# Kernel optimization log

Hardware: AMD Instinct MI355X
Metric: run time of the kernel (lower is better)

Reference implementation:

```python
import jax, jax.numpy as jnp
import numpy as np

V, C, T_MAX, H, L = 32000, 256, 2048, 8, 4
HS = C // H          # head_size = 32
FFN = 256            # hard-coded in Encoder
CLS_H, N_OUT = 512, 10
B, T = 4, 2048
EPS = 1e-5


def _ln(x, g, b):
    mu = jnp.mean(x, axis=-1, keepdims=True)
    var = jnp.mean(jnp.square(x - mu), axis=-1, keepdims=True)
    return (x - mu) * jax.lax.rsqrt(var + EPS) * g + b


def setup_inputs() -> dict:
    key = jax.random.key(0)
    ks = jax.random.split(key, 16)
    s = 0.02
    return {
        "idx": jax.random.randint(ks[0], (B, T), 0, V),
        "tok_emb": jax.random.normal(ks[1], (V, C), jnp.float32) * s,
        "pos_emb": jax.random.normal(ks[2], (T_MAX, C), jnp.float32) * s,
        "Wq": jax.random.normal(ks[3], (L, H, C, HS), jnp.float32) * s,
        "Wk": jax.random.normal(ks[4], (L, H, C, HS), jnp.float32) * s,
        "Wv": jax.random.normal(ks[5], (L, H, C, HS), jnp.float32) * s,
        "Wproj": jax.random.normal(ks[6], (L, C, C), jnp.float32) * s,
        "bproj": jnp.zeros((L, C), jnp.float32),
        "ln1_g": jnp.ones((L, C), jnp.float32), "ln1_b": jnp.zeros((L, C), jnp.float32),
        "ln2_g": jnp.ones((L, C), jnp.float32), "ln2_b": jnp.zeros((L, C), jnp.float32),
        "W1": jax.random.normal(ks[7], (L, C, FFN), jnp.float32) * s,
        "b1": jnp.zeros((L, FFN), jnp.float32),
        "W2": jax.random.normal(ks[8], (L, FFN, C), jnp.float32) * s,
        "b2": jnp.zeros((L, C), jnp.float32),
        "lnf_g": jnp.ones((C,), jnp.float32), "lnf_b": jnp.zeros((C,), jnp.float32),
        "Wc1": jax.random.normal(ks[9], (C, CLS_H), jnp.float32) * s,
        "bc1": jnp.zeros((CLS_H,), jnp.float32),
        "Wc2": jax.random.normal(ks[10], (CLS_H, N_OUT), jnp.float32) * s,
        "bc2": jnp.zeros((N_OUT,), jnp.float32),
    }


def reference(idx, tok_emb, pos_emb, Wq, Wk, Wv, Wproj, bproj,
              ln1_g, ln1_b, ln2_g, ln2_b, W1, b1, W2, b2,
              lnf_g, lnf_b, Wc1, bc1, Wc2, bc2):
    Bc, Tc = idx.shape
    x = tok_emb[idx] + pos_emb[:Tc]                       # [B,T,C]
    scale = C ** (-0.5)                                   # NOTE: scales by n_embd, not head_size (faithful)
    for i in range(L):
        h = _ln(x, ln1_g[i], ln1_b[i])
        q = jnp.einsum('btc,hcd->bhtd', h, Wq[i])
        k = jnp.einsum('btc,hcd->bhtd', h, Wk[i])
        v = jnp.einsum('btc,hcd->bhtd', h, Wv[i])
        wei = jax.nn.softmax(jnp.einsum('bhtd,bhsd->bhts', q, k) * scale, axis=-1)
        o = jnp.einsum('bhts,bhsd->bhtd', wei, v)         # [B,H,T,HS]
        o = o.transpose(0, 2, 1, 3).reshape(Bc, Tc, C)    # concat heads
        x = x + jnp.einsum('btc,cd->btd', o, Wproj[i]) + bproj[i]
        h2 = _ln(x, ln2_g[i], ln2_b[i])
        f = jax.nn.relu(jnp.einsum('btc,cf->btf', h2, W1[i]) + b1[i])
        x = x + jnp.einsum('btf,fc->btc', f, W2[i]) + b2[i]
    x = _ln(x, lnf_g, lnf_b)
    emb = jnp.mean(x, axis=1)                             # [B,C] mean pool over T
    logits = jax.nn.relu(emb @ Wc1 + bc1) @ Wc2 + bc2
    return jax.nn.softmax(logits, axis=1)                 # [B, n_output]
```

## Files before the change

kernel.cpp:

```cpp
#include <hip/hip_runtime.h>
#include <hip/hip_bf16.h>

#define NTOK 8192
#define CDIM 256
#define TDIM 2048
#define BDIM 4
#define HDIM 8
#define HSZ  32
#define LNUM 4
#define BUF  (NTOK*CDIM)
#define QSTR 768
#define LC   0.0901684400056f

typedef __attribute__((ext_vector_type(8))) short short8v;
typedef __attribute__((ext_vector_type(4))) short short4v;
typedef __attribute__((ext_vector_type(4))) float float4v;

#if __has_builtin(__builtin_amdgcn_cvt_pk_bf16_f32)
static __device__ __forceinline__ unsigned pkbf(float a, float b){
  auto t = __builtin_amdgcn_cvt_pk_bf16_f32(a, b);
  union { decltype(t) v; unsigned u; } cv; cv.v = t;
  return cv.u;
}
static __device__ __forceinline__ short f2bs(float f){
  auto t = __builtin_amdgcn_cvt_pk_bf16_f32(f, f);
  union { decltype(t) v; unsigned u; } cv; cv.v = t;
  return (short)(cv.u & 0xFFFFu);
}
#else
static __device__ __forceinline__ short f2bs(float f){
  union { float f; unsigned u; } x; x.f = f;
  unsigned r = x.u + 0x7FFFu + ((x.u >> 16) & 1u);
  return (short)(r >> 16);
}
static __device__ __forceinline__ unsigned pkbf(float a, float b){
  union { float f; unsigned u; } x, y; x.f = a; y.f = b;
  unsigned ra = x.u + 0x7FFFu + ((x.u >> 16) & 1u);
  unsigned rb = y.u + 0x7FFFu + ((y.u >> 16) & 1u);
  return __builtin_amdgcn_perm(rb, ra, 0x07060302u);
}
#endif
#if __has_builtin(__builtin_amdgcn_exp2f)
static __device__ __forceinline__ float fexp2(float x){ return __builtin_amdgcn_exp2f(x); }
#else
static __device__ __forceinline__ float fexp2(float x){ return __expf(x*0.6931471805599453f); }
#endif

#if __has_builtin(__builtin_amdgcn_mfma_f32_16x16x16bf16_1k)
static __device__ __forceinline__ float4v mfma16(short4v a, short4v b, float4v c){
  return __builtin_amdgcn_mfma_f32_16x16x16bf16_1k(a, b, c, 0, 0, 0);
}
#else
static __device__ __forceinline__ float4v mfma16(short4v a, short4v b, float4v c){
  float4v d;
  asm volatile("v_mfma_f32_16x16x16_bf16 %0, %1, %2, %3\n\ts_nop 7\n\ts_nop 7"
               : "=v"(d) : "v"(a), "v"(b), "v"(c));
  return d;
}
#endif
static __device__ __forceinline__ float4v mfma32(short8v a, short8v b, float4v c){
  return __builtin_amdgcn_mfma_f32_16x16x32_bf16(a, b, c, 0, 0, 0);
}

__global__ __launch_bounds__(256) void k_prep_embed(
    const int* __restrict__ idx, const float* __restrict__ tok, const float* __restrict__ pos,
    const float* __restrict__ Wq, const float* __restrict__ Wk, const float* __restrict__ Wv,
    const float* __restrict__ Wp, const float* __restrict__ W1, const float* __restrict__ W2,
    const float* __restrict__ l1g, const float* __restrict__ l2g,
    const float* __restrict__ l1b, const float* __restrict__ l2b,
    const float* __restrict__ b1, const float* __restrict__ Wc1, const float* __restrict__ lnfg,
    const float* __restrict__ lnfb, const float* __restrict__ bc1,
    short* __restrict__ qkvT, short* __restrict__ wpT, short* __restrict__ w1T, short* __restrict__ w2T,
    float* __restrict__ bq, float* __restrict__ b1f, float* __restrict__ Wc1s, float* __restrict__ bc1f,
    float* __restrict__ x, short* __restrict__ y) {
  const int tid = threadIdx.x;
  const int id = blockIdx.x;
  if (id >= 513) {
    const int bid = id - 513;
    const int lane = tid & 63;
    const int bt = bid*4 + (tid >> 6);
    const int t = bt & (TDIM-1);
    float4 tv = *(const float4*)&tok[(size_t)idx[bt]*CDIM + lane*4];
    float4 pv = *(const float4*)&pos[(size_t)t*CDIM + lane*4];
    float4 v = make_float4(tv.x+pv.x, tv.y+pv.y, tv.z+pv.z, tv.w+pv.w);
    *(float4*)&x[(size_t)bt*CDIM + lane*4] = v;
    float s1 = (v.x+v.y) + (v.z+v.w);
    float s2 = fmaf(v.x,v.x, fmaf(v.y,v.y, fmaf(v.z,v.z, v.w*v.w)));
    #pragma unroll
    for (int off=32; off>0; off>>=1) { s1 += __shfl_xor(s1, off, 64); s2 += __shfl_xor(s2, off, 64); }
    float mean = s1*(1.f/CDIM);
    float inv  = rsqrtf(s2*(1.f/CDIM) - mean*mean + 1e-5f);
    float cc = -mean*inv;
    union { unsigned u[2]; short4v s; } o;
    o.u[0] = pkbf(fmaf(v.x,inv,cc), fmaf(v.y,inv,cc));
    o.u[1] = pkbf(fmaf(v.z,inv,cc), fmaf(v.w,inv,cc));
    *(short4v*)&y[(size_t)bt*CDIM + lane*4] = o.s;
    return;
  }
  if (id < 384) {
    __shared__ float tile[64][65];
    int l = id / 96, rr = id % 96;
    const float* src; short* dst; int n0, k0; bool qkvmode; int gsel; float nscale = 1.f;
    if (rr < 48) {
      int tn = rr >> 2, tk = rr & 3;
      n0 = tn*64; k0 = tk*64;
      const float* b3 = (n0 < 256) ? Wq : (n0 < 512 ? Wk : Wv);
      src = b3 + l*65536;
      dst = qkvT + (size_t)l*QSTR*256;
      qkvmode = true; gsel = 1;
      if (n0 < 256) nscale = LC;
    } else {
      int r2 = rr - 48;
      int mat = r2 >> 4, t = r2 & 15;
      int tn = t >> 2, tk = t & 3;
      n0 = tn*64; k0 = tk*64;
      const float* b3 = (mat == 0) ? Wp : (mat == 1 ? W1 : W2);
      src = b3 + l*65536;
      dst = (mat == 0 ? wpT : (mat == 1 ? w1T : w2T)) + l*65536;
      qkvmode = false; gsel = (mat == 1) ? 2 : 0;
    }
    const int cn = tid & 63, rk = tid >> 6;
    #pragma unroll
    for (int i = 0; i < 16; ++i) {
      int kk = rk + i*4;
      int n = n0 + cn, k = k0 + kk;
      float v;
      if (qkvmode) { int nn = n & 255; v = src[((nn>>5)*256 + k)*32 + (nn & 31)]; }
      else         { v = src[k*256 + n]; }
      if (gsel == 1)      v *= l1g[l*256 + k];
      else if (gsel == 2) v *= l2g[l*256 + k];
      tile[kk][cn] = v;
    }
    __syncthreads();
    #pragma unroll
    for (int i = 0; i < 16; ++i) {
      int nn = rk + i*4;
      dst[(size_t)(n0 + nn)*256 + k0 + cn] = f2bs(tile[cn][nn] * nscale);
    }
  } else if (id < 448) {
    __shared__ float red[4][64];
    int bid = id - 384;
    int l = bid >> 4, seg = bid & 15;
    int o = seg*64 + (tid & 63), pp = tid >> 6;
    float s = 0.f;
    if (o < 768) {
      const float* W = (o < 256 ? Wq : (o < 512 ? Wk : Wv)) + l*65536;
      int nn = o & 255, h = nn >> 5, d = nn & 31;
      const float* bv = l1b + l*256;
      for (int k = pp*64; k < pp*64+64; ++k) s = fmaf(bv[k], W[(h*256 + k)*32 + d], s);
    } else {
      const float* W = W1 + l*65536;
      int n = o - 768;
      const float* bv = l2b + l*256;
      for (int k = pp*64; k < pp*64+64; ++k) s = fmaf(bv[k], W[k*256 + n], s);
    }
    red[pp][tid & 63] = s;
    __syncthreads();
    if (tid < 64) {
      float tot = red[0][tid]+red[1][tid]+red[2][tid]+red[3][tid];
      int oo = seg*64 + tid;
      if (oo < 768) bq[l*768 + oo] = tot * (oo < 256 ? LC : 1.f);
      else          b1f[l*256 + (oo-768)] = b1[l*256 + (oo-768)] + tot;
    }
  } else if (id < 512) {
    int base = (id-448)*2048;
    #pragma unroll
    for (int i=0;i<8;++i) {
      int idx2 = base + i*256 + tid;
      Wc1s[idx2] = Wc1[idx2] * lnfg[idx2 >> 9];
    }
  } else {
    for (int u = tid; u < 512; u += 256) {
      float s = bc1[u];
      for (int k=0;k<256;++k) s = fmaf(lnfb[k], Wc1[k*512+u], s);
      bc1f[u] = s;
    }
  }
}

template<int NF, bool BIAS, bool RELU, bool OUTBF16, bool ACCUM>
__global__ __launch_bounds__(64) void k_gemm3(const short* __restrict__ A,
    const short* __restrict__ Bt, const float* __restrict__ bias, void* __restrict__ Cv,
    int outstride) {
  const int lane = threadIdx.x;
  const int q4 = lane >> 4, r = lane & 15;
  const int blockRow = blockIdx.x * 32;
  const int blockCol = blockIdx.y * (NF*16);
  float4v acc[2][NF];
  #pragma unroll
  for (int i=0;i<2;++i)
    #pragma unroll
    for (int j=0;j<NF;++j) acc[i][j] = (float4v){0,0,0,0};
  #pragma unroll
  for (int k0 = 0; k0 < 256; k0 += 32) {
    short8v a0 = *(const short8v*)&A[(size_t)(blockRow +      r)*CDIM + k0 + q4*8];
    short8v a1 = *(const short8v*)&A[(size_t)(blockRow + 16 + r)*CDIM + k0 + q4*8];
    #pragma unroll
    for (int nf=0; nf<NF; ++nf) {
      short8v bf = *(const short8v*)&Bt[(size_t)(blockCol + nf*16 + r)*256 + k0 + q4*8];
      acc[0][nf] = mfma32(a0, bf, acc[0][nf]);
      acc[1][nf] = mfma32(a1, bf, acc[1][nf]);
    }
  }
  #pragma unroll
  for (int mf=0; mf<2; ++mf)
    #pragma unroll
    for (int nf=0; nf<NF; ++nf) {
      int col = blockCol + nf*16 + r;
      float bb = BIAS ? bias[col] : 0.f;
      #pragma unroll
      for (int reg=0; reg<4; ++reg) {
        int row = blockRow + mf*16 + q4*4 + reg;
        float v = acc[mf][nf][reg] + bb;
        if (RELU) v = fmaxf(v, 0.f);
        size_t oi = (size_t)row*outstride + col;
        if (ACCUM)        ((float*)Cv)[oi] += v;
        else if (OUTBF16) ((short*)Cv)[oi] = f2bs(v);
        else              ((float*)Cv)[oi] = v;
      }
    }
}

template<bool LAST>
__global__ __launch_bounds__(512, 4) void k_mlp(
    const short* __restrict__ A,
    const short* __restrict__ Bt,
    const float* __restrict__ bias,
    const short* __restrict__ W1t, const float* __restrict__ b1f,
    const short* __restrict__ W2t, const float* __restrict__ b2,
    float* __restrict__ X,
    const short* __restrict__ Wqkv,
    const float* __restrict__ bq,
    short* __restrict__ Qout) {
  __shared__ __align__(16) short Ys[16*264];
  __shared__ __align__(16) short Gs[16*264];
  __shared__ float S1[16][8], S2[16][8];
  const int tid = threadIdx.x;
  const int w = tid >> 6, lane = tid & 63;
  const int q4 = lane >> 4, r = lane & 15;
  const int row0 = blockIdx.x * 16;
  const int col0 = w*32;
  float4v acc[2];
  float xv[2][4];

  acc[0] = (float4v){0,0,0,0}; acc[1] = (float4v){0,0,0,0};
  #pragma unroll
  for (int k=0;k<8;++k) {
    short8v a0 = *(const short8v*)&A[(size_t)(row0 + r)*CDIM + k*32 + q4*8];
    short8v b0 = *(const short8v*)&Bt[(size_t)(col0 +      r)*256 + k*32 + q4*8];
    short8v b1r= *(const short8v*)&Bt[(size_t)(col0 + 16 + r)*256 + k*32 + q4*8];
    acc[0] = mfma32(a0, b0,  acc[0]);
    acc[1] = mfma32(a0, b1r, acc[1]);
  }
  {
    float sw1[4], sw2[4];
    #pragma unroll
    for (int reg=0; reg<4; ++reg) {
      int row = row0 + q4*4 + reg;
      float s1 = 0.f, s2 = 0.f;
      #pragma unroll
      for (int nf=0; nf<2; ++nf) {
        int col = col0 + nf*16 + r;
        float t = acc[nf][reg] + bias[col] + X[(size_t)row*CDIM + col];
        xv[nf][reg] = t;
        s1 += t; s2 = fmaf(t, t, s2);
      }
      #pragma unroll
      for (int off=1; off<16; off<<=1) { s1 += __shfl_xor(s1, off, 64); s2 += __shfl_xor(s2, off, 64); }
      sw1[reg] = s1; sw2[reg] = s2;
    }
    if (r == 0) {
      #pragma unroll
      for (int reg=0; reg<4; ++reg) {
        S1[q4*4 + reg][w] = sw1[reg];
        S2[q4*4 + reg][w] = sw2[reg];
      }
    }
    __syncthreads();
    #pragma unroll
    for (int reg=0; reg<4; ++reg) {
      int ri = q4*4 + reg;
      float s1 = ((S1[ri][0]+S1[ri][1]) + (S1[ri][2]+S1[ri][3]))
               + ((S1[ri][4]+S1[ri][5]) + (S1[ri][6]+S1[ri][7]));
      float s2 = ((S2[ri][0]+S2[ri][1]) + (S2[ri][2]+S2[ri][3]))
               + ((S2[ri][4]+S2[ri][5]) + (S2[ri][6]+S2[ri][7]));
      float mean = s1*(1.f/CDIM);
      float inv  = rsqrtf(s2*(1.f/CDIM) - mean*mean + 1e-5f);
      float cc = -mean*inv;
      #pragma unroll
      for (int nf=0; nf<2; ++nf) {
        int col = col0 + nf*16 + r;
        Ys[ri*264 + col] = f2bs(fmaf(xv[nf][reg], inv, cc));
      }
    }
  }
  __syncthreads();

  acc[0] = (float4v){0,0,0,0}; acc[1] = (float4v){0,0,0,0};
  #pragma unroll
  for (int k=0;k<8;++k) {
    short8v a0 = *(const short8v*)&Ys[(r)*264 + k*32 + q4*8];
    short8v b0 = *(const short8v*)&W1t[(size_t)(col0 +      r)*256 + k*32 + q4*8];
    short8v b1r= *(const short8v*)&W1t[(size_t)(col0 + 16 + r)*256 + k*32 + q4*8];
    acc[0] = mfma32(a0, b0,  acc[0]);
    acc[1] = mfma32(a0, b1r, acc[1]);
  }
  #pragma unroll
  for (int nf=0; nf<2; ++nf) {
    int col = col0 + nf*16 + r;
    float bb = b1f[col];
    #pragma unroll
    for (int reg=0; reg<4; ++reg) {
      int rl = q4*4 + reg;
      Gs[rl*264 + col] = f2bs(fmaxf(acc[nf][reg] + bb, 0.f));
    }
  }
  __syncthreads();
  acc[0] = (float4v){0,0,0,0}; acc[1] = (float4v){0,0,0,0};
  #pragma unroll
  for (int k=0;k<8;++k) {
    short8v a0 = *(const short8v*)&Gs[(r)*264 + k*32 + q4*8];
    short8v b0 = *(const short8v*)&W2t[(size_t)(col0 +      r)*256 + k*32 + q4*8];
    short8v b1r= *(const short8v*)&W2t[(size_t)(col0 + 16 + r)*256 + k*32 + q4*8];
    acc[0] = mfma32(a0, b0,  acc[0]);
    acc[1] = mfma32(a0, b1r, acc[1]);
  }
  {
    float sw1[4], sw2[4];
    #pragma unroll
    for (int reg=0; reg<4; ++reg) {
      int row = row0 + q4*4 + reg;
      float s1 = 0.f, s2 = 0.f;
      #pragma unroll
      for (int nf=0; nf<2; ++nf) {
        int col = col0 + nf*16 + r;
        float t = acc[nf][reg] + b2[col] + xv[nf][reg];
        xv[nf][reg] = t;
        X[(size_t)row*CDIM + col] = t;
        s1 += t; s2 = fmaf(t, t, s2);
      }
      if (!LAST) {
        #pragma unroll
        for (int off=1; off<16; off<<=1) { s1 += __shfl_xor(s1, off, 64); s2 += __shfl_xor(s2, off, 64); }
        sw1[reg] = s1; sw2[reg] = s2;
      }
    }
    if (LAST) return;
    if (r == 0) {
      #pragma unroll
      for (int reg=0; reg<4; ++reg) {
        S1[q4*4 + reg][w] = sw1[reg];
        S2[q4*4 + reg][w] = sw2[reg];
      }
    }
    __syncthreads();
    #pragma unroll
    for (int reg=0; reg<4; ++reg) {
      int ri = q4*4 + reg;
      float s1 = ((S1[ri][0]+S1[ri][1]) + (S1[ri][2]+S1[ri][3]))
               + ((S1[ri][4]+S1[ri][5]) + (S1[ri][6]+S1[ri][7]));
      float s2 = ((S2[ri][0]+S2[ri][1]) + (S2[ri][2]+S2[ri][3]))
               + ((S2[ri][4]+S2[ri][5]) + (S2[ri][6]+S2[ri][7]));
      float mean = s1*(1.f/CDIM);
      float inv  = rsqrtf(s2*(1.f/CDIM) - mean*mean + 1e-5f);
      float cc = -mean*inv;
      #pragma unroll
      for (int nf=0; nf<2; ++nf) {
        int col = col0 + nf*16 + r;
        Ys[ri*264 + col] = f2bs(fmaf(xv[nf][reg], inv, cc));
      }
    }
  }
  __syncthreads();

  {
    const int cb = w*96;
    float4v qa[6];
    #pragma unroll
    for (int j=0;j<6;++j) qa[j] = (float4v){0,0,0,0};
    #pragma unroll
    for (int k=0;k<8;++k) {
      short8v a0 = *(const short8v*)&Ys[(r)*264 + k*32 + q4*8];
      #pragma unroll
      for (int nf=0; nf<6; ++nf) {
        short8v bf = *(const short8v*)&Wqkv[(size_t)(cb + nf*16 + r)*256 + k*32 + q4*8];
        qa[nf] = mfma32(a0, bf, qa[nf]);
      }
    }
    #pragma unroll
    for (int nf=0; nf<6; ++nf) {
      int col = cb + nf*16 + r;
      float bb = bq[col];
      #pragma unroll
      for (int reg=0; reg<4; ++reg) {
        int row = row0 + q4*4 + reg;
        Qout[(size_t)row*QSTR + col] = f2bs(qa[nf][reg] + bb);
      }
    }
  }
}

#define KSS 40
#define VTS 140
__global__ __launch_bounds__(512) void k_attn6(const short* __restrict__ qkv,
    short* __restrict__ O) {
  __shared__ __align__(16) short Ks[2][128*KSS];
  __shared__ __align__(16) short Vt[2][32*VTS];
  const int tid = threadIdx.x;
  const int w = tid >> 6, lane = tid & 63;
  const int q4 = lane >> 4, r = lane & 15;
  const int b = blockIdx.z, h = blockIdx.y;
  const int rowbase = blockIdx.x*128 + w*16;
  short8v Qf = *(const short8v*)&qkv[((size_t)(b*TDIM + rowbase + r))*QSTR + h*HSZ + q4*8];
  float4v o0 = {0,0,0,0}, o1 = {0,0,0,0};
  float l0 = 0.f;
  const bool isV = tid >= 256;
  const int t2 = tid & 255;
  const int kkey = t2 >> 1, kd0 = (t2 & 1)*16;
  const int kp = t2 & 63, dg = t2 >> 6;
  const short* kvbase = qkv + (size_t)b*TDIM*QSTR + h*HSZ;
  short8v ka, kb2, va, vb;
  if (isV) {
    va = *(const short8v*)&kvbase[(size_t)(2*kp)*QSTR   + 2*CDIM + dg*8];
    vb = *(const short8v*)&kvbase[(size_t)(2*kp+1)*QSTR + 2*CDIM + dg*8];
  } else {
    ka  = *(const short8v*)&kvbase[(size_t)kkey*QSTR + CDIM + kd0];
    kb2 = *(const short8v*)&kvbase[(size_t)kkey*QSTR + CDIM + kd0 + 8];
  }
  int p = 0;
  for (int s0 = 0; s0 < TDIM; s0 += 128, p ^= 1) {
    if (isV) {
      union { short8v s; unsigned u[4]; } A, C;
      A.s = va; C.s = vb;
      #pragma unroll
      for (int j=0;j<4;++j) {
        *(unsigned*)&Vt[p][(dg*8+2*j  )*VTS + 2*kp] = __builtin_amdgcn_perm(C.u[j], A.u[j], 0x05040100u);
        *(unsigned*)&Vt[p][(dg*8+2*j+1)*VTS + 2*kp] = __builtin_amdgcn_perm(C.u[j], A.u[j], 0x07060302u);
      }
    } else {
      *(short8v*)&Ks[p][kkey*KSS + kd0]     = ka;
      *(short8v*)&Ks[p][kkey*KSS + kd0 + 8] = kb2;
    }
    if (s0 + 128 < TDIM) {
      const short* nb = kvbase + (size_t)(s0+128)*QSTR;
      if (isV) {
        va = *(const short8v*)&nb[(size_t)(2*kp)*QSTR   + 2*CDIM + dg*8];
        vb = *(const short8v*)&nb[(size_t)(2*kp+1)*QSTR + 2*CDIM + dg*8];
      } else {
        ka  = *(const short8v*)&nb[(size_t)kkey*QSTR + CDIM + kd0];
        kb2 = *(const short8v*)&nb[(size_t)kkey*QSTR + CDIM + kd0 + 8];
      }
    }
    __syncthreads();
    #pragma unroll
    for (int ks = 0; ks < 8; ++ks) {
      short8v Kf = *(const short8v*)&Ks[p][(ks*16 + r)*KSS + q4*8];
      float4v sv = mfma32(Kf, Qf, (float4v){0,0,0,0});
      short4v Vf0 = *(const short4v*)&Vt[p][r*VTS + ks*16 + q4*4];
      short4v Vf1 = *(const short4v*)&Vt[p][(16+r)*VTS + ks*16 + q4*4];
      float p0 = fexp2(sv[0]), p1 = fexp2(sv[1]);
      float p2 = fexp2(sv[2]), p3 = fexp2(sv[3]);
      l0 += (p0+p1) + (p2+p3);
      union { unsigned u[2]; short4v s; } P;
      P.u[0] = pkbf(p0, p1); P.u[1] = pkbf(p2, p3);
      o0 = mfma16(P.s, Vf0, o0);
      o1 = mfma16(P.s, Vf1, o1);
    }
  }
  l0 += __shfl_xor(l0, 16, 64); l0 += __shfl_xor(l0, 32, 64);
  #pragma unroll
  for (int reg=0; reg<4; ++reg) {
    int qrow = q4*4 + reg;
    float i0 = 1.f / __shfl(l0, qrow, 64);
    short* op = O + ((size_t)(b*TDIM + rowbase + qrow))*CDIM + h*HSZ;
    op[r]    = f2bs(o0[reg]*i0);
    op[16+r] = f2bs(o1[reg]*i0);
  }
}

__global__ __launch_bounds__(256) void k_poolln(const float* __restrict__ X, float* __restrict__ part) {
  __shared__ float red[4][256];
  int b = blockIdx.x >> 3, chunk = blockIdx.x & 7;
  int wv = threadIdx.x >> 6, lane = threadIdx.x & 63;
  int base = b*TDIM + chunk*256 + wv*64;
  float a0=0,a1=0,a2=0,a3=0;
  for (int rr=0; rr<64; ++rr) {
    float4 v = *(const float4*)&X[(size_t)(base+rr)*CDIM + lane*4];
    float s1 = (v.x+v.y)+(v.z+v.w);
    float s2 = fmaf(v.x,v.x, fmaf(v.y,v.y, fmaf(v.z,v.z, v.w*v.w)));
    #pragma unroll
    for (int off=32; off>0; off>>=1) { s1 += __shfl_xor(s1,off,64); s2 += __shfl_xor(s2,off,64); }
    float mean = s1*(1.f/256.f);
    float inv  = rsqrtf(s2*(1.f/256.f) - mean*mean + 1e-5f);
    a0 = fmaf(v.x-mean, inv, a0); a1 = fmaf(v.y-mean, inv, a1);
    a2 = fmaf(v.z-mean, inv, a2); a3 = fmaf(v.w-mean, inv, a3);
  }
  red[wv][lane*4+0]=a0; red[wv][lane*4+1]=a1; red[wv][lane*4+2]=a2; red[wv][lane*4+3]=a3;
  __syncthreads();
  int c = threadIdx.x;
  part[blockIdx.x*256 + c] = (red[0][c]+red[1][c]+red[2][c]+red[3][c]) * (1.f/2048.f);
}

__global__ __launch_bounds__(512) void k_cls(const float* __restrict__ part,
    const float* __restrict__ Wc1s, const float* __restrict__ bc1f,
    const float* __restrict__ Wc2, const float* __restrict__ bc2, float* __restrict__ out) {
  __shared__ float se[4][256];
  __shared__ float sh[4][512];
  __shared__ float red[160];
  __shared__ float sl[40];
  const int t = threadIdx.x;
  for (int j=t; j<1024; j+=512) {
    int b = j >> 8, c = j & 255;
    float s = 0.f;
    #pragma unroll
    for (int ch=0; ch<8; ++ch) s += part[(b*8+ch)*256 + c];
    se[b][c] = s;
  }
  __syncthreads();
  {
    float bb = bc1f[t];
    float a0=bb, a1=bb, a2=bb, a3=bb;
    for (int c=0; c<256; ++c) {
      float w2 = Wc1s[c*512 + t];
      a0 = fmaf(se[0][c], w2, a0); a1 = fmaf(se[1][c], w2, a1);
      a2 = fmaf(se[2][c], w2, a2); a3 = fmaf(se[3][c], w2, a3);
    }
    sh[0][t]=fmaxf(a0,0.f); sh[1][t]=fmaxf(a1,0.f);
    sh[2][t]=fmaxf(a2,0.f); sh[3][t]=fmaxf(a3,0.f);
  }
  __syncthreads();
  if (t < 160) {
    int o = t >> 2, pp = t & 3;
    int b = o / 10, j = o - b*10;
    const float* hp = &sh[b][pp*128];
    float s = 0.f;
    #pragma unroll 8
    for (int u=0; u<128; ++u) s = fmaf(hp[u], Wc2[(pp*128+u)*10 + j], s);
    red[t] = s;
  }
  __syncthreads();
  if (t < 40) sl[t] = (red[t*4]+red[t*4+1]) + (red[t*4+2]+red[t*4+3]) + bc2[t%10];
  __syncthreads();
  if (t < 4) {
    float mx = -1e30f;
    for (int j=0;j<10;++j) mx = fmaxf(mx, sl[t*10+j]);
    float e[10], sum = 0.f;
    for (int j=0;j<10;++j) { e[j] = __expf(sl[t*10+j]-mx); sum += e[j]; }
    float inv = 1.f/sum;
    for (int j=0;j<10;++j) out[t*10+j] = e[j]*inv;
  }
}

extern "C" void kernel_launch(void* const* d_in, const int* in_sizes, int n_in,
                              void* d_out, int out_size, void* d_ws, size_t ws_size,
                              hipStream_t stream) {
  const int*   idx = (const int*)d_in[0];
  const float* tok = (const float*)d_in[1];
  const float* pos = (const float*)d_in[2];
  const float* Wq  = (const float*)d_in[3];
  const float* Wk  = (const float*)d_in[4];
  const float* Wv  = (const float*)d_in[5];
  const float* Wp  = (const float*)d_in[6];
  const float* bp  = (const float*)d_in[7];
  const float* l1g = (const float*)d_in[8];
  const float* l1b = (const float*)d_in[9];
  const float* l2g = (const float*)d_in[10];
  const float* l2b = (const float*)d_in[11];
  const float* W1  = (const float*)d_in[12];
  const float* b1  = (const float*)d_in[13];
  const float* W2  = (const float*)d_in[14];
  const float* b2  = (const float*)d_in[15];
  const float* lfg = (const float*)d_in[16];
  const float* lfb = (const float*)d_in[17];
  const float* Wc1 = (const float*)d_in[18];
  const float* bc1 = (const float*)d_in[19];
  const float* Wc2 = (const float*)d_in[20];
  const float* bc2 = (const float*)d_in[21];

  char* p = (char*)d_ws;
  float* xb   = (float*)p;              p += (size_t)BUF*4;
  short* hb   = (short*)p;              p += (size_t)BUF*2;
  short* qkvb = (short*)p;              p += (size_t)NTOK*QSTR*2;
  float* part = (float*)p;              p += 32*256*4;
  short* wqkvT = (short*)p;             p += (size_t)LNUM*QSTR*256*2;
  short* wpT   = (short*)p;             p += (size_t)LNUM*65536*2;
  short* w1T   = (short*)p;             p += (size_t)LNUM*65536*2;
  short* w2T   = (short*)p;             p += (size_t)LNUM*65536*2;
  float* bq    = (float*)p;             p += (size_t)LNUM*768*4;
  float* b1f   = (float*)p;             p += (size_t)LNUM*256*4;
  float* Wc1s  = (float*)p;             p += (size_t)256*512*4;
  float* bc1f  = (float*)p;             p += 512*4;

  k_prep_embed<<<513 + NTOK/4, 256, 0, stream>>>(idx, tok, pos,
                                   Wq, Wk, Wv, Wp, W1, W2, l1g, l2g, l1b, l2b,
                                   b1, Wc1, lfg, lfb, bc1,
                                   wqkvT, wpT, w1T, w2T, bq, b1f, Wc1s, bc1f,
                                   xb, hb);
  k_gemm3<4,true,false,true,false><<<dim3(256,12), 64, 0, stream>>>(
      hb, wqkvT, bq, qkvb, QSTR);
  for (int l = 0; l < LNUM; ++l) {
    k_attn6<<<dim3(16, HDIM, BDIM), 512, 0, stream>>>(qkvb, hb);
    if (l < LNUM-1) {
      k_mlp<false><<<512, 512, 0, stream>>>(
          hb, wpT + (size_t)l*65536, bp + l*CDIM,
          w1T + (size_t)l*65536, b1f + l*CDIM, w2T + (size_t)l*65536, b2 + l*CDIM,
          xb,
          wqkvT + (size_t)(l+1)*QSTR*256, bq + (l+1)*768, qkvb);
    } else {
      k_mlp<true><<<512, 512, 0, stream>>>(
          hb, wpT + (size_t)l*65536, bp + l*CDIM,
          w1T + (size_t)l*65536, b1f + l*CDIM, w2T + (size_t)l*65536, b2 + l*CDIM,
          xb,
          wqkvT, bq, qkvb);
    }
  }
  k_poolln<<<32, 256, 0, stream>>>(xb, part);
  k_cls<<<1, 512, 0, stream>>>(part, Wc1s, bc1f, Wc2, bc2, (float*)d_out);
}
```

Measured before the change: 532.4 us.

## Pre-swizzle weights into MFMA fragment layout and widen MLP blocks to 32 rows

Weights are now stored in a fragment-tiled layout during prep, so each lane's B operand is one contiguous 16-byte load and each wave reads a fully coalesced 1 KB chunk. The fused MLP kernel moves from 16 rows per 512-thread block to 32 rows per 1024-thread block, with 16 waves each owning a 16-column slice. Each weight fragment is reused across two row tiles, and the activation tile is staged once in shared memory. This halves weight traffic per row. In exchange, the LayerNorm reduction goes through more partial sums, and 1024-thread blocks put more pressure on occupancy.

```diff
diff --git a/kernel.cpp b/kernel.cpp
--- a/kernel.cpp
+++ b/kernel.cpp
@@ -60,6 +60,10 @@
 #endif
 static __device__ __forceinline__ float4v mfma32(short8v a, short8v b, float4v c){
   return __builtin_amdgcn_mfma_f32_16x16x32_bf16(a, b, c, 0, 0, 0);
+}
+
+static __device__ __forceinline__ int faddr(int n, int k){
+  return ((n>>4)*8 + (k>>5))*512 + ((((k>>3)&3)<<4) + (n&15))*8 + (k&7);
 }
 
 __global__ __launch_bounds__(256) void k_prep_embed(
@@ -135,7 +139,7 @@
     #pragma unroll
     for (int i = 0; i < 16; ++i) {
       int nn = rk + i*4;
-      dst[(size_t)(n0 + nn)*256 + k0 + cn] = f2bs(tile[cn][nn] * nscale);
+      dst[faddr(n0 + nn, k0 + cn)] = f2bs(tile[cn][nn] * nscale);
     }
   } else if (id < 448) {
     __shared__ float red[4][64];
@@ -197,7 +201,7 @@
     short8v a1 = *(const short8v*)&A[(size_t)(blockRow + 16 + r)*CDIM + k0 + q4*8];
     #pragma unroll
     for (int nf=0; nf<NF; ++nf) {
-      short8v bf = *(const short8v*)&Bt[(size_t)(blockCol + nf*16 + r)*256 + k0 + q4*8];
+      short8v bf = *(const short8v*)&Bt[(size_t)(((blockCol>>4) + nf)*8 + (k0>>5))*512 + lane*8];
       acc[0][nf] = mfma32(a0, bf, acc[0][nf]);
       acc[1][nf] = mfma32(a1, bf, acc[1][nf]);
     }
@@ -222,7 +226,7 @@
 }
 
 template<bool LAST>
-__global__ __launch_bounds__(512, 4) void k_mlp(
+__global__ __launch_bounds__(1024, 4) void k_mlp(
     const short* __restrict__ A,
     const short* __restrict__ Bt,
     const float* __restrict__ bias,
@@ -232,169 +236,157 @@
     const short* __restrict__ Wqkv,
     const float* __restrict__ bq,
     short* __restrict__ Qout) {
-  __shared__ __align__(16) short Ys[16*264];
-  __shared__ __align__(16) short Gs[16*264];
-  __shared__ float S1[16][8], S2[16][8];
+  __shared__ __align__(16) short Ys[32*264];
+  __shared__ __align__(16) short Gs[32*264];
+  __shared__ float S1[32][16], S2[32][16];
   const int tid = threadIdx.x;
   const int w = tid >> 6, lane = tid & 63;
   const int q4 = lane >> 4, r = lane & 15;
-  const int row0 = blockIdx.x * 16;
-  const int col0 = w*32;
-  float4v acc[2];
-  float xv[2][4];
-
-  acc[0] = (float4v){0,0,0,0}; acc[1] = (float4v){0,0,0,0};
+  const int row0 = blockIdx.x * 32;
+  const int colw = w*16 + r;
+
+  {
+    short8v av = *(const short8v*)&A[(size_t)row0*CDIM + tid*8];
+    *(short8v*)&Gs[(tid>>5)*264 + (tid&31)*8] = av;
+  }
+  __syncthreads();
+
+  float4v acc0 = {0,0,0,0}, acc1 = {0,0,0,0};
   #pragma unroll
   for (int k=0;k<8;++k) {
-    short8v a0 = *(const short8v*)&A[(size_t)(row0 + r)*CDIM + k*32 + q4*8];
-    short8v b0 = *(const short8v*)&Bt[(size_t)(col0 +      r)*256 + k*32 + q4*8];
-    short8v b1r= *(const short8v*)&Bt[(size_t)(col0 + 16 + r)*256 + k*32 + q4*8];
-    acc[0] = mfma32(a0, b0,  acc[0]);
-    acc[1] = mfma32(a0, b1r, acc[1]);
-  }
+    short8v b  = *(const short8v*)&Bt[(size_t)(w*8+k)*512 + lane*8];
+    short8v a0 = *(const short8v*)&Gs[(     r)*264 + k*32 + q4*8];
+    short8v a1 = *(const short8v*)&Gs[(16 + r)*264 + k*32 + q4*8];
+    acc0 = mfma32(a0, b, acc0);
+    acc1 = mfma32(a1, b, acc1);
+  }
+  float xv0[4], xv1[4];
   {
-    float sw1[4], sw2[4];
+    float bb = bias[colw];
     #pragma unroll
     for (int reg=0; reg<4; ++reg) {
-      int row = row0 + q4*4 + reg;
-      float s1 = 0.f, s2 = 0.f;
+      float t0 = acc0[reg] + bb + X[(size_t)(row0 +      q4*4 + reg)*CDIM + colw];
+      float t1 = acc1[reg] + bb + X[(size_t)(row0 + 16 + q4*4 + reg)*CDIM + colw];
+      xv0[reg] = t0; xv1[reg] = t1;
+      float s10 = t0, s20 = t0*t0, s11 = t1, s21 = t1*t1;
       #pragma unroll
-      for (int nf=0; nf<2; ++nf) {
-        int col = col0 + nf*16 + r;
-        float t = acc[nf][reg] + bias[col] + X[(size_t)row*CDIM + col];
-        xv[nf][reg] = t;
-        s1 += t; s2 = fmaf(t, t, s2);
-      }
+      for (int off=1; off<16; off<<=1) {
+        s10 += __shfl_xor(s10, off, 64); s20 += __shfl_xor(s20, off, 64);
+        s11 += __shfl_xor(s11, off, 64); s21 += __shfl_xor(s21, off, 64);
+      }
+      if (r == 0) {
+        S1[     q4*4 + reg][w] = s10; S2[     q4*4 + reg][w] = s20;
+        S1[16 + q4*4 + reg][w] = s11; S2[16 + q4*4 + reg][w] = s21;
+      }
+    }
+  }
+  __syncthreads();
+  #pragma unroll
+  for (int reg=0; reg<4; ++reg) {
+    int r0i = q4*4 + reg, r1i = 16 + q4*4 + reg;
+    float s1=0.f, s2=0.f, t1=0.f, t2=0.f;
+    #pragma unroll
+    for (int j=0;j<16;++j) { s1 += S1[r0i][j]; s2 += S2[r0i][j]; t1 += S1[r1i][j]; t2 += S2[r1i][j]; }
+    float mean = s1*(1.f/CDIM);
+    float inv  = rsqrtf(s2*(1.f/CDIM) - mean*mean + 1e-5f);
+    Ys[r0i*264 + colw] = f2bs(fmaf(xv0[reg], inv, -mean*inv));
+    float mean2 = t1*(1.f/CDIM);
+    float inv2  = rsqrtf(t2*(1.f/CDIM) - mean2*mean2 + 1e-5f);
+    Ys[r1i*264 + colw] = f2bs(fmaf(xv1[reg], inv2, -mean2*inv2));
+  }
+  __syncthreads();
+
+  acc0 = (float4v){0,0,0,0}; acc1 = (float4v){0,0,0,0};
+  #pragma unroll
+  for (int k=0;k<8;++k) {
+    short8v b  = *(const short8v*)&W1t[(size_t)(w*8+k)*512 + lane*8];
+    short8v a0 = *(const short8v*)&Ys[(     r)*264 + k*32 + q4*8];
+    short8v a1 = *(const short8v*)&Ys[(16 + r)*264 + k*32 + q4*8];
+    acc0 = mfma32(a0, b, acc0);
+    acc1 = mfma32(a1, b, acc1);
+  }
+  {
+    float g = b1f[colw];
+    #pragma unroll
+    for (int reg=0; reg<4; ++reg) {
+      Gs[(     q4*4 + reg)*264 + colw] = f2bs(fmaxf(acc0[reg] + g, 0.f));
+      Gs[(16 + q4*4 + reg)*264 + colw] = f2bs(fmaxf(acc1[reg] + g, 0.f));
+    }
+  }
+  __syncthreads();
+
+  acc0 = (float4v){0,0,0,0}; acc1 = (float4v){0,0,0,0};
+  #pragma unroll
+  for (int k=0;k<8;++k) {
+    short8v b  = *(const short8v*)&W2t[(size_t)(w*8+k)*512 + lane*8];
+    short8v a0 = *(const short8v*)&Gs[(     r)*264 + k*32 + q4*8];
+    short8v a1 = *(const short8v*)&Gs[(16 + r)*264 + k*32 + q4*8];
+    acc0 = mfma32(a0, b, acc0);
+    acc1 = mfma32(a1, b, acc1);
+  }
+  {
+    float bb2 = b2[colw];
+    #pragma unroll
+    for (int reg=0; reg<4; ++reg) {
+      float t0 = acc0[reg] + bb2 + xv0[reg];
+      float t1 = acc1[reg] + bb2 + xv1[reg];
+      xv0[reg] = t0; xv1[reg] = t1;
+      X[(size_t)(row0 +      q4*4 + reg)*CDIM + colw] = t0;
+      X[(size_t)(row0 + 16 + q4*4 + reg)*CDIM + colw] = t1;
+      if (!LAST) {
+        float s10 = t0, s20 = t0*t0, s11 = t1, s21 = t1*t1;
+        #pragma unroll
+        for (int off=1; off<16; off<<=1) {
+          s10 += __shfl_xor(s10, off, 64); s20 += __shfl_xor(s20, off, 64);
+          s11 += __shfl_xor(s11, off, 64); s21 += __shfl_xor(s21, off, 64);
+        }
+        if (r == 0) {
+          S1[     q4*4 + reg][w] = s10; S2[     q4*4 + reg][w] = s20;
+          S1[16 + q4*4 + reg][w] = s11; S2[16 + q4*4 + reg][w] = s21;
+        }
+      }
+    }
+  }
+  if (LAST) return;
+  __syncthreads();
+  #pragma unroll
+  for (int reg=0; reg<4; ++reg) {
+    int r0i = q4*4 + reg, r1i = 16 + q4*4 + reg;
+    float s1=0.f, s2=0.f, t1=0.f, t2=0.f;
+    #pragma unroll
+    for (int j=0;j<16;++j) { s1 += S1[r0i][j]; s2 += S2[r0i][j]; t1 += S1[r1i][j]; t2 += S2[r1i][j]; }
+    float mean = s1*(1.f/CDIM);
+    float inv  = rsqrtf(s2*(1.f/CDIM) - mean*mean + 1e-5f);
+    Ys[r0i*264 + colw] = f2bs(fmaf(xv0[reg], inv, -mean*inv));
+    float mean2 = t1*(1.f/CDIM);
+    float inv2  = rsqrtf(t2*(1.f/CDIM) - mean2*mean2 + 1e-5f);
+    Ys[r1i*264 + colw] = f2bs(fmaf(xv1[reg], inv2, -mean2*inv2));
+  }
+  __syncthreads();
+
+  {
+    float4v qa0[3], qa1[3];
+    #pragma unroll
+    for (int j=0;j<3;++j) { qa0[j] = (float4v){0,0,0,0}; qa1[j] = (float4v){0,0,0,0}; }
+    #pragma unroll
+    for (int k=0;k<8;++k) {
+      short8v ay0 = *(const short8v*)&Ys[(     r)*264 + k*32 + q4*8];
+      short8v ay1 = *(const short8v*)&Ys[(16 + r)*264 + k*32 + q4*8];
       #pragma unroll
-      for (int off=1; off<16; off<<=1) { s1 += __shfl_xor(s1, off, 64); s2 += __shfl_xor(s2, off, 64); }
-      sw1[reg] = s1; sw2[reg] = s2;
-    }
-    if (r == 0) {
-      #pragma unroll
-      for (int reg=0; reg<4; ++reg) {
-        S1[q4*4 + reg][w] = sw1[reg];
-        S2[q4*4 + reg][w] = sw2[reg];
-      }
-    }
-    __syncthreads();
-    #pragma unroll
-    for (int reg=0; reg<4; ++reg) {
-      int ri = q4*4 + reg;
-      float s1 = ((S1[ri][0]+S1[ri][1]) + (S1[ri][2]+S1[ri][3]))
-               + ((S1[ri][4]+S1[ri][5]) + (S1[ri][6]+S1[ri][7]));
-      float s2 = ((S2[ri][0]+S2[ri][1]) + (S2[ri][2]+S2[ri][3]))
-               + ((S2[ri][4]+S2[ri][5]) + (S2[ri][6]+S2[ri][7]));
-      float mean = s1*(1.f/CDIM);
-      float inv  = rsqrtf(s2*(1.f/CDIM) - mean*mean + 1e-5f);
-      float cc = -mean*inv;
-      #pragma unroll
-      for (int nf=0; nf<2; ++nf) {
-        int col = col0 + nf*16 + r;
-        Ys[ri*264 + col] = f2bs(fmaf(xv[nf][reg], inv, cc));
-      }
-    }
-  }
-  __syncthreads();
-
-  acc[0] = (float4v){0,0,0,0}; acc[1] = (float4v){0,0,0,0};
-  #pragma unroll
-  for (int k=0;k<8;++k) {
-    short8v a0 = *(const short8v*)&Ys[(r)*264 + k*32 + q4*8];
-    short8v b0 = *(const short8v*)&W1t[(size_t)(col0 +      r)*256 + k*32 + q4*8];
-    short8v b1r= *(const short8v*)&W1t[(size_t)(col0 + 16 + r)*256 + k*32 + q4*8];
-    acc[0] = mfma32(a0, b0,  acc[0]);
-    acc[1] = mfma32(a0, b1r, acc[1]);
-  }
-  #pragma unroll
-  for (int nf=0; nf<2; ++nf) {
-    int col = col0 + nf*16 + r;
-    float bb = b1f[col];
-    #pragma unroll
-    for (int reg=0; reg<4; ++reg) {
-      int rl = q4*4 + reg;
-      Gs[rl*264 + col] = f2bs(fmaxf(acc[nf][reg] + bb, 0.f));
-    }
-  }
-  __syncthreads();
-  acc[0] = (float4v){0,0,0,0}; acc[1] = (float4v){0,0,0,0};
-  #pragma unroll
-  for (int k=0;k<8;++k) {
-    short8v a0 = *(const short8v*)&Gs[(r)*264 + k*32 + q4*8];
-    short8v b0 = *(const short8v*)&W2t[(size_t)(col0 +      r)*256 + k*32 + q4*8];
-    short8v b1r= *(const short8v*)&W2t[(size_t)(col0 + 16 + r)*256 + k*32 + q4*8];
-    acc[0] = mfma32(a0, b0,  acc[0]);
-    acc[1] = mfma32(a0, b1r, acc[1]);
-  }
-  {
-    float sw1[4], sw2[4];
-    #pragma unroll
-    for (int reg=0; reg<4; ++reg) {
-      int row = row0 + q4*4 + reg;
-      float s1 = 0.f, s2 = 0.f;
-      #pragma unroll
-      for (int nf=0; nf<2; ++nf) {
-        int col = col0 + nf*16 + r;
-        float t = acc[nf][reg] + b2[col] + xv[nf][reg];
-        xv[nf][reg] = t;
-        X[(size_t)row*CDIM + col] = t;
-        s1 += t; s2 = fmaf(t, t, s2);
-      }
-      if (!LAST) {
-        #pragma unroll
-        for (int off=1; off<16; off<<=1) { s1 += __shfl_xor(s1, off, 64); s2 += __shfl_xor(s2, off, 64); }
-        sw1[reg] = s1; sw2[reg] = s2;
-      }
-    }
-    if (LAST) return;
-    if (r == 0) {
-      #pragma unroll
-      for (int reg=0; reg<4; ++reg) {
-        S1[q4*4 + reg][w] = sw1[reg];
-        S2[q4*4 + reg][w] = sw2[reg];
-      }
-    }
-    __syncthreads();
-    #pragma unroll
-    for (int reg=0; reg<4; ++reg) {
-      int ri = q4*4 + reg;
-      float s1 = ((S1[ri][0]+S1[ri][1]) + (S1[ri][2]+S1[ri][3]))
-               + ((S1[ri][4]+S1[ri][5]) + (S1[ri][6]+S1[ri][7]));
-      float s2 = ((S2[ri][0]+S2[ri][1]) + (S2[ri][2]+S2[ri][3]))
-               + ((S2[ri][4]+S2[ri][5]) + (S2[ri][6]+S2[ri][7]));
-      float mean = s1*(1.f/CDIM);
-      float inv  = rsqrtf(s2*(1.f/CDIM) - mean*mean + 1e-5f);
-      float cc = -mean*inv;
-      #pragma unroll
-      for (int nf=0; nf<2; ++nf) {
-        int col = col0 + nf*16 + r;
-        Ys[ri*264 + col] = f2bs(fmaf(xv[nf][reg], inv, cc));
-      }
-    }
-  }
-  __syncthreads();
-
-  {
-    const int cb = w*96;
-    float4v qa[6];
-    #pragma unroll
-    for (int j=0;j<6;++j) qa[j] = (float4v){0,0,0,0};
-    #pragma unroll
-    for (int k=0;k<8;++k) {
-      short8v a0 = *(const short8v*)&Ys[(r)*264 + k*32 + q4*8];
-      #pragma unroll
-      for (int nf=0; nf<6; ++nf) {
-        short8v bf = *(const short8v*)&Wqkv[(size_t)(cb + nf*16 + r)*256 + k*32 + q4*8];
-        qa[nf] = mfma32(a0, bf, qa[nf]);
-      }
-    }
-    #pragma unroll
-    for (int nf=0; nf<6; ++nf) {
-      int col = cb + nf*16 + r;
+      for (int nf=0; nf<3; ++nf) {
+        short8v b = *(const short8v*)&Wqkv[(size_t)((w*3+nf)*8 + k)*512 + lane*8];
+        qa0[nf] = mfma32(ay0, b, qa0[nf]);
+        qa1[nf] = mfma32(ay1, b, qa1[nf]);
+      }
+    }
+    #pragma unroll
+    for (int nf=0; nf<3; ++nf) {
+      int col = (w*3+nf)*16 + r;
       float bb = bq[col];
       #pragma unroll
       for (int reg=0; reg<4; ++reg) {
-        int row = row0 + q4*4 + reg;
-        Qout[(size_t)row*QSTR + col] = f2bs(qa[nf][reg] + bb);
+        Qout[(size_t)(row0 +      q4*4 + reg)*QSTR + col] = f2bs(qa0[nf][reg] + bb);
+        Qout[(size_t)(row0 + 16 + q4*4 + reg)*QSTR + col] = f2bs(qa1[nf][reg] + bb);
       }
     }
   }
@@ -601,13 +593,13 @@
   for (int l = 0; l < LNUM; ++l) {
     k_attn6<<<dim3(16, HDIM, BDIM), 512, 0, stream>>>(qkvb, hb);
     if (l < LNUM-1) {
-      k_mlp<false><<<512, 512, 0, stream>>>(
+      k_mlp<false><<<256, 1024, 0, stream>>>(
           hb, wpT + (size_t)l*65536, bp + l*CDIM,
           w1T + (size_t)l*65536, b1f + l*CDIM, w2T + (size_t)l*65536, b2 + l*CDIM,
           xb,
           wqkvT + (size_t)(l+1)*QSTR*256, bq + (l+1)*768, qkvb);
     } else {
-      k_mlp<true><<<512, 512, 0, stream>>>(
+      k_mlp<true><<<256, 1024, 0, stream>>>(
           hb, wpT + (size_t)l*65536, bp + l*CDIM,
           w1T + (size_t)l*65536, b1f + l*CDIM, w2T + (size_t)l*65536, b2 + l*CDIM,
           xb,
```

Measured after the change: 461.3 us. 13.4% less time.
